# Optimization experiments

Hardware: AMD Instinct MI355X
Metric: run time of the kernel (lower is better)

Reference implementation:

```python
import jax, jax.numpy as jnp
import numpy as np

B, T, C, H = 2, 2048, 1024, 16
D = C // H  # head_dim = 64

def setup_inputs() -> dict:
    key = jax.random.key(0)
    k1, k2, k3, k4, k5 = jax.random.split(key, 5)
    x = jax.random.normal(k1, (B, T, C), dtype=jnp.float32)
    # RoPE tables (realistic frequencies)
    inv_freq = 1.0 / (10000.0 ** (jnp.arange(0, D // 2, dtype=jnp.float32) / (D // 2)))
    pos = jnp.arange(T, dtype=jnp.float32)
    ang = pos[:, None] * inv_freq[None, :]          # (T, D/2)
    cos, sin = jnp.cos(ang), jnp.sin(ang)
    # causal mask (True = keep)
    mask = jnp.tril(jnp.ones((T, T), dtype=bool))
    W_qkv = jax.random.normal(k2, (3 * C, C), dtype=jnp.float32) * (1.0 / np.sqrt(C))
    W_out = jax.random.normal(k3, (C, C), dtype=jnp.float32) * (1.0 / np.sqrt(C))
    return {"x": x, "cos": cos, "sin": sin, "mask": mask, "W_qkv": W_qkv, "W_out": W_out}

def apply_rope(x, cos, sin):
    # x: (B, H, T, D); cos/sin: (T, D/2)
    d = x.shape[-1] // 2
    x1, x2 = x[..., :d], x[..., d:]
    c = cos[None, None, :x.shape[2], :]
    s = sin[None, None, :x.shape[2], :]
    return jnp.concatenate([x1 * c - x2 * s, x2 * c + x1 * s], axis=-1)

def reference(x, cos, sin, mask, W_qkv, W_out):
    b, t, c = x.shape
    qkv = (x @ W_qkv.T).reshape(b, t, 3, H, D)
    q, k, v = qkv[:, :, 0], qkv[:, :, 1], qkv[:, :, 2]   # (b, t, H, D)
    q = q.transpose(0, 2, 1, 3)
    k = k.transpose(0, 2, 1, 3)
    v = v.transpose(0, 2, 1, 3)                           # (b, H, t, D)
    q = apply_rope(q, cos, sin)
    k = apply_rope(k, cos, sin)
    attn = jnp.einsum('bhqd,bhkd->bhqk', q, k) / jnp.sqrt(jnp.asarray(D, x.dtype))
    attn = jnp.where(mask[None, None, :, :], attn, -jnp.inf)
    attn = jax.nn.softmax(attn, axis=-1)
    out = jnp.einsum('bhqk,bhkd->bhqd', attn, v)          # (b, H, t, D)
    out = out.transpose(0, 2, 1, 3).reshape(b, t, c)
    return out @ W_out.T
```

## Files before the change

### kernel.cpp

```cpp
#include <hip/hip_runtime.h>
#include <stdint.h>

typedef __bf16 bf16;
typedef __bf16 bf16x4 __attribute__((ext_vector_type(4)));
typedef __bf16 bf16x8 __attribute__((ext_vector_type(8)));
typedef float f32x4 __attribute__((ext_vector_type(4)));

#define TSEQ 2048
#define NHEAD 16
#define HDIM 64
#define CDIM 1024

#define AS1(p) ((const __attribute__((address_space(1))) void*)(p))
#define AS3(p) ((__attribute__((address_space(3))) void*)(p))

#if __has_builtin(__builtin_amdgcn_exp2f)
#define EXP2(x) __builtin_amdgcn_exp2f(x)
#else
#define EXP2(x) exp2f(x)
#endif

__global__ __launch_bounds__(256) void cast3_bf16(const float* __restrict__ in1, int n1,
                                                  const float* __restrict__ in2, int n2,
                                                  const float* __restrict__ in3, int n3,
                                                  bf16* __restrict__ out1,
                                                  bf16* __restrict__ out2,
                                                  bf16* __restrict__ out3) {
  int i = (blockIdx.x * 256 + threadIdx.x) * 8;
  const float* src;
  bf16* dst;
  if (i < n1) {
    src = in1 + i; dst = out1 + i;
  } else if (i < n1 + n2) {
    src = in2 + (i - n1); dst = out2 + (i - n1);
  } else if (i < n1 + n2 + n3) {
    src = in3 + (i - n1 - n2); dst = out3 + (i - n1 - n2);
  } else {
    return;
  }
  float4 a = *(const float4*)src;
  float4 b = *(const float4*)(src + 4);
  bf16x8 r;
  r[0] = (bf16)a.x; r[1] = (bf16)a.y; r[2] = (bf16)a.z; r[3] = (bf16)a.w;
  r[4] = (bf16)b.x; r[5] = (bf16)b.y; r[6] = (bf16)b.z; r[7] = (bf16)b.w;
  *(bf16x8*)dst = r;
}

__global__ __launch_bounds__(256) void gemm_qkv_rope(const bf16* __restrict__ A,
                                                     const bf16* __restrict__ B,
                                                     const float* __restrict__ cosb,
                                                     const float* __restrict__ sinb,
                                                     bf16* __restrict__ Qb,
                                                     bf16* __restrict__ Kb,
                                                     bf16* __restrict__ Vt) {
  constexpr int K = 1024;
  __shared__ bf16 smem[8704];
  const int t = threadIdx.x;
  const int w = t >> 6, l = t & 63, g = l >> 4, ln = l & 15;
  const int wm = (w >> 1) * 64, wn = (w & 1) * 64;
  const int m0 = blockIdx.x * 128, n0 = blockIdx.y * 128;
  const int r0 = t >> 2, kc0 = (t & 3) * 8;

  f32x4 acc[4][4] = {};

  for (int k0 = 0; k0 < K; k0 += 32) {
    __syncthreads();
    __builtin_amdgcn_global_load_lds(AS1(A + (size_t)(m0 + r0) * K + k0 + kc0),
                                     AS3(&smem[t * 8]), 16, 0, 0);
    __builtin_amdgcn_global_load_lds(AS1(A + (size_t)(m0 + r0 + 64) * K + k0 + kc0),
                                     AS3(&smem[(t + 256) * 8]), 16, 0, 0);
    __builtin_amdgcn_global_load_lds(AS1(B + (size_t)(n0 + r0) * K + k0 + kc0),
                                     AS3(&smem[4096 + t * 8]), 16, 0, 0);
    __builtin_amdgcn_global_load_lds(AS1(B + (size_t)(n0 + r0 + 64) * K + k0 + kc0),
                                     AS3(&smem[4096 + (t + 256) * 8]), 16, 0, 0);
    __syncthreads();
    bf16x8 af[4], bfr[4];
#pragma unroll
    for (int i = 0; i < 4; i++) {
      af[i] = *(const bf16x8*)&smem[(wm + i * 16 + ln) * 32 + g * 8];
      bfr[i] = *(const bf16x8*)&smem[4096 + (wn + i * 16 + ln) * 32 + g * 8];
    }
#pragma unroll
    for (int i = 0; i < 4; i++)
#pragma unroll
      for (int j = 0; j < 4; j++)
        acc[i][j] = __builtin_amdgcn_mfma_f32_16x16x32_bf16(af[i], bfr[j], acc[i][j], 0, 0, 0);
  }

  const int part = n0 >> 10;
  if (part < 2) {
    bf16* dst = part ? Kb : Qb;
    const float qs = part ? 1.0f : 0.18033688011112042f;
#pragma unroll
    for (int i = 0; i < 4; i++)
#pragma unroll
      for (int j = 0; j < 2; j++) {
        int nl = (n0 & 1023) + wn + j * 16 + ln;
        int h = nl >> 6, d = nl & 31;
#pragma unroll
        for (int r = 0; r < 4; r++) {
          int row = m0 + wm + i * 16 + g * 4 + r;
          int tok = row & (TSEQ - 1), bb = row >> 11;
          float c = cosb[tok * 32 + d], s = sinb[tok * 32 + d];
          float a1 = acc[i][j][r], a2 = acc[i][j + 2][r];
          size_t ob = ((size_t)(bb * NHEAD + h) * TSEQ + tok) * HDIM + d;
          dst[ob] = (bf16)((a1 * c - a2 * s) * qs);
          dst[ob + 32] = (bf16)((a2 * c + a1 * s) * qs);
        }
      }
  } else {
    const int bb = m0 >> 11;
    const int tbase = m0 & (TSEQ - 1);
    const int nbase = n0 - 2048;
#pragma unroll
    for (int pass = 0; pass < 2; pass++) {
      __syncthreads();
      if ((w >> 1) == pass) {
#pragma unroll
        for (int i = 0; i < 4; i++)
#pragma unroll
          for (int j = 0; j < 4; j++) {
            int lr = i * 16 + g * 4;
            int lc = wn + j * 16 + ln;
#pragma unroll
            for (int r = 0; r < 4; r++)
              smem[(lr + r) * 132 + lc] = (bf16)acc[i][j][r];
          }
      }
      __syncthreads();
      for (int c = t; c < 1024; c += 256) {
        int ch = c >> 3, tc = c & 7;
        bf16x8 o;
#pragma unroll
        for (int j2 = 0; j2 < 8; j2++) o[j2] = smem[(tc * 8 + j2) * 132 + ch];
        int n = nbase + ch;
        int h = n >> 6, d = n & 63;
        *(bf16x8*)(Vt + ((size_t)((bb * NHEAD + h) * HDIM + d)) * TSEQ +
                   tbase + pass * 64 + tc * 8) = o;
      }
    }
  }
}

__global__ __launch_bounds__(256) void gemm_out(const bf16* __restrict__ A,
                                                const bf16* __restrict__ B,
                                                float* __restrict__ C,
                                                int M, int N, int K) {
  __shared__ bf16 As[64 * 32];
  __shared__ bf16 Bs[128 * 32];
  const int t = threadIdx.x;
  const int w = t >> 6, l = t & 63, g = l >> 4, ln = l & 15;
  const int m0 = blockIdx.x * 64, n0 = blockIdx.y * 128;
  const int r0 = t >> 2, kc0 = (t & 3) * 8;

  f32x4 acc[4][2] = {};

  for (int k0 = 0; k0 < K; k0 += 32) {
    __syncthreads();
    __builtin_amdgcn_global_load_lds(AS1(A + (size_t)(m0 + r0) * K + k0 + kc0),
                                     AS3(&As[t * 8]), 16, 0, 0);
    __builtin_amdgcn_global_load_lds(AS1(B + (size_t)(n0 + r0) * K + k0 + kc0),
                                     AS3(&Bs[t * 8]), 16, 0, 0);
    __builtin_amdgcn_global_load_lds(AS1(B + (size_t)(n0 + r0 + 64) * K + k0 + kc0),
                                     AS3(&Bs[(t + 256) * 8]), 16, 0, 0);
    __syncthreads();
    bf16x8 af[4], bfr[2];
#pragma unroll
    for (int i = 0; i < 4; i++)
      af[i] = *(const bf16x8*)&As[(i * 16 + ln) * 32 + g * 8];
#pragma unroll
    for (int j = 0; j < 2; j++)
      bfr[j] = *(const bf16x8*)&Bs[(w * 32 + j * 16 + ln) * 32 + g * 8];
#pragma unroll
    for (int i = 0; i < 4; i++)
#pragma unroll
      for (int j = 0; j < 2; j++)
        acc[i][j] = __builtin_amdgcn_mfma_f32_16x16x32_bf16(af[i], bfr[j], acc[i][j], 0, 0, 0);
  }
#pragma unroll
  for (int i = 0; i < 4; i++)
#pragma unroll
    for (int j = 0; j < 2; j++) {
      int row = m0 + i * 16 + g * 4;
      int col = n0 + w * 32 + j * 16 + ln;
#pragma unroll
      for (int r = 0; r < 4; r++)
        C[(size_t)(row + r) * N + col] = acc[i][j][r];
    }
}

__global__ __launch_bounds__(256) void attn_fwd(const bf16* __restrict__ Q,
                                                const bf16* __restrict__ K,
                                                const bf16* __restrict__ Vt,
                                                bf16* __restrict__ ctx) {
  __shared__ bf16 Ks[2][64 * 64];
  __shared__ bf16 VTs[2][64 * 64];
  __shared__ bf16 Ps[4][2][16 * 64];

  const int t = threadIdx.x;
  const int w = t >> 6;
  const int l = t & 63, g = l >> 4, ln = l & 15;
  const int bid = blockIdx.x;
  const int bh = bid & 31;
  const int qb0 = 15 - (bid >> 5);
  const size_t base = (size_t)bh * TSEQ * HDIM;

  const int q0 = qb0 * 128;
  const int qwb = q0 + w * 32;
  const int dtile = qwb >> 6;
  const int ktmax = 2 * qb0 + 1;
  const int lswz = (ln & 7) * 8;

  const int r0 = t >> 3, ch0 = (t & 7) * 8;
  const int sx = ((t & 7) ^ (r0 & 7)) * 8;
  const int s0 = r0 * 64 + sx;
  const int s1 = (r0 + 32) * 64 + sx;

  bf16x8 bq[2][2];
#pragma unroll
  for (int qs = 0; qs < 2; qs++) {
    const int q_g = qwb + qs * 16 + ln;
    bq[qs][0] = *(const bf16x8*)(Q + base + (size_t)q_g * HDIM + g * 8);
    bq[qs][1] = *(const bf16x8*)(Q + base + (size_t)q_g * HDIM + 32 + g * 8);
  }

  const bf16* kp0 = K + base + (size_t)r0 * HDIM + ch0;
  const bf16* kp1 = kp0 + 32 * HDIM;
  const bf16* vp0 = Vt + base + (size_t)r0 * TSEQ + ch0;
  const bf16* vp1 = vp0 + 32 * TSEQ;
  bf16x8 kr0 = *(const bf16x8*)kp0;
  bf16x8 kr1 = *(const bf16x8*)kp1;
  bf16x8 vr0 = *(const bf16x8*)vp0;
  bf16x8 vr1 = *(const bf16x8*)vp1;

  f32x4 acc[2][4] = {};
  float l_run[2] = {0.f, 0.f};

  for (int kt = 0; kt <= ktmax; kt++) {
    bf16* ks = Ks[kt & 1];
    bf16* vs = VTs[kt & 1];
    *(bf16x8*)&ks[s0] = kr0;
    *(bf16x8*)&ks[s1] = kr1;
    *(bf16x8*)&vs[s0] = vr0;
    *(bf16x8*)&vs[s1] = vr1;
    __syncthreads();
    if (kt < ktmax) {
      kr0 = *(const bf16x8*)(kp0 + (size_t)(kt + 1) * 64 * HDIM);
      kr1 = *(const bf16x8*)(kp1 + (size_t)(kt + 1) * 64 * HDIM);
      vr0 = *(const bf16x8*)(vp0 + (kt + 1) * 64);
      vr1 = *(const bf16x8*)(vp1 + (kt + 1) * 64);
    }
    if (kt <= dtile) {
      f32x4 st[2][4] = {};
      __builtin_amdgcn_s_setprio(1);
#pragma unroll
      for (int step = 0; step < 2; step++)
#pragma unroll
        for (int mt = 0; mt < 4; mt++) {
          bf16x8 ak = *(const bf16x8*)&ks[(mt * 16 + ln) * 64 + ((step * 32 + g * 8) ^ lswz)];
          st[0][mt] = __builtin_amdgcn_mfma_f32_16x16x32_bf16(ak, bq[0][step], st[0][mt], 0, 0, 0);
          st[1][mt] = __builtin_amdgcn_mfma_f32_16x16x32_bf16(ak, bq[1][step], st[1][mt], 0, 0, 0);
        }
      __builtin_amdgcn_s_setprio(0);
#pragma unroll
      for (int qs2 = 0; qs2 < 2; qs2++) {
        const int q_g = qwb + qs2 * 16 + ln;
        float vals[16];
        if (kt == dtile) {
#pragma unroll
          for (int mt = 0; mt < 4; mt++)
#pragma unroll
            for (int r = 0; r < 4; r++) {
              int kg = kt * 64 + mt * 16 + g * 4 + r;
              vals[mt * 4 + r] = (kg <= q_g) ? st[qs2][mt][r] : -INFINITY;
            }
        } else {
#pragma unroll
          for (int mt = 0; mt < 4; mt++)
#pragma unroll
            for (int r = 0; r < 4; r++) vals[mt * 4 + r] = st[qs2][mt][r];
        }
        float psum = 0.f;
#pragma unroll
        for (int i2 = 0; i2 < 16; i2++) {
          float p = EXP2(vals[i2]);
          vals[i2] = p;
          psum += p;
        }
        psum += __shfl_xor(psum, 16);
        psum += __shfl_xor(psum, 32);
        l_run[qs2] += psum;
#pragma unroll
        for (int mt = 0; mt < 4; mt++) {
          bf16x4 pk;
#pragma unroll
          for (int r = 0; r < 4; r++) pk[r] = (bf16)vals[mt * 4 + r];
          *(bf16x4*)&Ps[w][qs2][ln * 64 + (((mt * 16 + (g >> 1) * 8) ^ lswz) + (g & 1) * 4)] = pk;
        }
      }
      __builtin_amdgcn_s_setprio(1);
#pragma unroll
      for (int step = 0; step < 2; step++) {
        bf16x8 ap0 = *(const bf16x8*)&Ps[w][0][ln * 64 + ((step * 32 + g * 8) ^ lswz)];
        bf16x8 ap1 = *(const bf16x8*)&Ps[w][1][ln * 64 + ((step * 32 + g * 8) ^ lswz)];
#pragma unroll
        for (int nt = 0; nt < 4; nt++) {
          bf16x8 bv = *(const bf16x8*)&vs[(nt * 16 + ln) * 64 + ((step * 32 + g * 8) ^ lswz)];
          acc[0][nt] = __builtin_amdgcn_mfma_f32_16x16x32_bf16(ap0, bv, acc[0][nt], 0, 0, 0);
          acc[1][nt] = __builtin_amdgcn_mfma_f32_16x16x32_bf16(ap1, bv, acc[1][nt], 0, 0, 0);
        }
      }
      __builtin_amdgcn_s_setprio(0);
    }
  }

  const int b = bh >> 4, h = bh & (NHEAD - 1);
#pragma unroll
  for (int qs2 = 0; qs2 < 2; qs2++) {
    float inv = 1.0f / l_run[qs2];
    float lrow[4];
#pragma unroll
    for (int r = 0; r < 4; r++) lrow[r] = __shfl(inv, g * 4 + r, 64);
#pragma unroll
    for (int nt = 0; nt < 4; nt++)
#pragma unroll
      for (int r = 0; r < 4; r++) {
        int q = qwb + qs2 * 16 + g * 4 + r;
        ctx[(size_t)(b * TSEQ + q) * CDIM + h * HDIM + nt * 16 + ln] =
            (bf16)(acc[qs2][nt][r] * lrow[r]);
      }
  }
}

extern "C" void kernel_launch(void* const* d_in, const int* in_sizes, int n_in,
                              void* d_out, int out_size, void* d_ws, size_t ws_size,
                              hipStream_t stream) {
  const float* x = (const float*)d_in[0];
  const float* cosb = (const float*)d_in[1];
  const float* sinb = (const float*)d_in[2];
  const float* Wqkv = (const float*)d_in[4];
  const float* Wout = (const float*)d_in[5];
  float* out = (float*)d_out;

  char* ws = (char*)d_ws;
  bf16* x_bf = (bf16*)ws;
  bf16* ctx = (bf16*)ws;
  bf16* Wqkv_bf = (bf16*)(ws + 8388608);
  bf16* Wout_bf = (bf16*)(ws + 14680064);
  bf16* Qb = (bf16*)(ws + 16777216);
  bf16* Kb = (bf16*)(ws + 25165824);
  bf16* Vt = (bf16*)(ws + 33554432);

  cast3_bf16<<<(4194304 + 3145728 + 1048576) / 8 / 256, 256, 0, stream>>>(
      x, 4194304, Wqkv, 3145728, Wout, 1048576, x_bf, Wqkv_bf, Wout_bf);
  gemm_qkv_rope<<<dim3(32, 24), 256, 0, stream>>>(x_bf, Wqkv_bf, cosb, sinb, Qb, Kb, Vt);
  attn_fwd<<<512, 256, 0, stream>>>(Qb, Kb, Vt, ctx);
  gemm_out<<<dim3(64, 8), 256, 0, stream>>>(ctx, Wout_bf, out, 4096, 1024, 1024);
}
```

Baseline: 196.3 us.

## Split attention KV loop across two wave groups per block and merge partials

The attention block grows from 256 to 512 threads. Two groups of four waves each process alternating 64-key tiles, so each block loads 128 keys per iteration into single-buffered shared memory. At the end the second group writes its partial accumulators and row sums to shared memory, and the first group adds them, normalizes and writes the output. The goal is to halve the serial key-loop length per query tile and raise wave parallelism. The cost is an extra barrier per iteration, losing the double buffer, 64KB of shared memory per block, and a reduction epilogue.

```diff
diff --git a/kernel.cpp b/kernel.cpp
--- a/kernel.cpp
+++ b/kernel.cpp
@@ -189,16 +189,21 @@
     }
 }
 
-__global__ __launch_bounds__(256) void attn_fwd(const bf16* __restrict__ Q,
-                                                const bf16* __restrict__ K,
-                                                const bf16* __restrict__ Vt,
-                                                bf16* __restrict__ ctx) {
-  __shared__ bf16 Ks[2][64 * 64];
-  __shared__ bf16 VTs[2][64 * 64];
-  __shared__ bf16 Ps[4][2][16 * 64];
+__global__ __launch_bounds__(512, 4) void attn_fwd(const bf16* __restrict__ Q,
+                                                   const bf16* __restrict__ K,
+                                                   const bf16* __restrict__ Vt,
+                                                   bf16* __restrict__ ctx) {
+  __shared__ __align__(16) char smem_raw[65536];
+  bf16* Ks = (bf16*)smem_raw;
+  bf16* VTs = (bf16*)(smem_raw + 16384);
+  bf16* Ps = (bf16*)(smem_raw + 32768);
+  float* Mbuf = (float*)smem_raw;
+  float* Lbuf = (float*)(smem_raw + 32768);
 
   const int t = threadIdx.x;
   const int w = t >> 6;
+  const int p = w >> 2;
+  const int qw = w & 3;
   const int l = t & 63, g = l >> 4, ln = l & 15;
   const int bid = blockIdx.x;
   const int bh = bid & 31;
@@ -206,13 +211,14 @@
   const size_t base = (size_t)bh * TSEQ * HDIM;
 
   const int q0 = qb0 * 128;
-  const int qwb = q0 + w * 32;
+  const int qwb = q0 + qw * 32;
   const int dtile = qwb >> 6;
-  const int ktmax = 2 * qb0 + 1;
   const int lswz = (ln & 7) * 8;
 
-  const int r0 = t >> 3, ch0 = (t & 7) * 8;
-  const int sx = ((t & 7) ^ (r0 & 7)) * 8;
+  const int ts = t >> 8;
+  const int tt = t & 255;
+  const int r0 = tt >> 3, ch0 = (tt & 7) * 8;
+  const int sx = ((tt & 7) ^ (r0 & 7)) * 8;
   const int s0 = r0 * 64 + sx;
   const int s1 = (r0 + 32) * 64 + sx;
 
@@ -224,9 +230,9 @@
     bq[qs][1] = *(const bf16x8*)(Q + base + (size_t)q_g * HDIM + 32 + g * 8);
   }
 
-  const bf16* kp0 = K + base + (size_t)r0 * HDIM + ch0;
+  const bf16* kp0 = K + base + (size_t)(ts * 64 + r0) * HDIM + ch0;
   const bf16* kp1 = kp0 + 32 * HDIM;
-  const bf16* vp0 = Vt + base + (size_t)r0 * TSEQ + ch0;
+  const bf16* vp0 = Vt + base + (size_t)r0 * TSEQ + ts * 64 + ch0;
   const bf16* vp1 = vp0 + 32 * TSEQ;
   bf16x8 kr0 = *(const bf16x8*)kp0;
   bf16x8 kr1 = *(const bf16x8*)kp1;
@@ -236,20 +242,20 @@
   f32x4 acc[2][4] = {};
   float l_run[2] = {0.f, 0.f};
 
-  for (int kt = 0; kt <= ktmax; kt++) {
-    bf16* ks = Ks[kt & 1];
-    bf16* vs = VTs[kt & 1];
-    *(bf16x8*)&ks[s0] = kr0;
-    *(bf16x8*)&ks[s1] = kr1;
-    *(bf16x8*)&vs[s0] = vr0;
-    *(bf16x8*)&vs[s1] = vr1;
-    __syncthreads();
-    if (kt < ktmax) {
-      kr0 = *(const bf16x8*)(kp0 + (size_t)(kt + 1) * 64 * HDIM);
-      kr1 = *(const bf16x8*)(kp1 + (size_t)(kt + 1) * 64 * HDIM);
-      vr0 = *(const bf16x8*)(vp0 + (kt + 1) * 64);
-      vr1 = *(const bf16x8*)(vp1 + (kt + 1) * 64);
-    }
+  for (int i = 0; i <= qb0; i++) {
+    __syncthreads();
+    *(bf16x8*)&Ks[ts * 4096 + s0] = kr0;
+    *(bf16x8*)&Ks[ts * 4096 + s1] = kr1;
+    *(bf16x8*)&VTs[ts * 4096 + s0] = vr0;
+    *(bf16x8*)&VTs[ts * 4096 + s1] = vr1;
+    __syncthreads();
+    if (i < qb0) {
+      kr0 = *(const bf16x8*)(kp0 + (size_t)(i + 1) * 128 * HDIM);
+      kr1 = *(const bf16x8*)(kp1 + (size_t)(i + 1) * 128 * HDIM);
+      vr0 = *(const bf16x8*)(vp0 + (i + 1) * 128);
+      vr1 = *(const bf16x8*)(vp1 + (i + 1) * 128);
+    }
+    const int kt = 2 * i + p;
     if (kt <= dtile) {
       f32x4 st[2][4] = {};
       __builtin_amdgcn_s_setprio(1);
@@ -257,7 +263,8 @@
       for (int step = 0; step < 2; step++)
 #pragma unroll
         for (int mt = 0; mt < 4; mt++) {
-          bf16x8 ak = *(const bf16x8*)&ks[(mt * 16 + ln) * 64 + ((step * 32 + g * 8) ^ lswz)];
+          bf16x8 ak = *(const bf16x8*)&Ks[p * 4096 + (mt * 16 + ln) * 64 +
+                                          ((step * 32 + g * 8) ^ lswz)];
           st[0][mt] = __builtin_amdgcn_mfma_f32_16x16x32_bf16(ak, bq[0][step], st[0][mt], 0, 0, 0);
           st[1][mt] = __builtin_amdgcn_mfma_f32_16x16x32_bf16(ak, bq[1][step], st[1][mt], 0, 0, 0);
         }
@@ -283,9 +290,9 @@
         float psum = 0.f;
 #pragma unroll
         for (int i2 = 0; i2 < 16; i2++) {
-          float p = EXP2(vals[i2]);
-          vals[i2] = p;
-          psum += p;
+          float pv = EXP2(vals[i2]);
+          vals[i2] = pv;
+          psum += pv;
         }
         psum += __shfl_xor(psum, 16);
         psum += __shfl_xor(psum, 32);
@@ -295,17 +302,21 @@
           bf16x4 pk;
 #pragma unroll
           for (int r = 0; r < 4; r++) pk[r] = (bf16)vals[mt * 4 + r];
-          *(bf16x4*)&Ps[w][qs2][ln * 64 + (((mt * 16 + (g >> 1) * 8) ^ lswz) + (g & 1) * 4)] = pk;
+          *(bf16x4*)&Ps[(w * 2 + qs2) * 1024 + ln * 64 +
+                        (((mt * 16 + (g >> 1) * 8) ^ lswz) + (g & 1) * 4)] = pk;
         }
       }
       __builtin_amdgcn_s_setprio(1);
 #pragma unroll
       for (int step = 0; step < 2; step++) {
-        bf16x8 ap0 = *(const bf16x8*)&Ps[w][0][ln * 64 + ((step * 32 + g * 8) ^ lswz)];
-        bf16x8 ap1 = *(const bf16x8*)&Ps[w][1][ln * 64 + ((step * 32 + g * 8) ^ lswz)];
+        bf16x8 ap0 = *(const bf16x8*)&Ps[(w * 2 + 0) * 1024 + ln * 64 +
+                                         ((step * 32 + g * 8) ^ lswz)];
+        bf16x8 ap1 = *(const bf16x8*)&Ps[(w * 2 + 1) * 1024 + ln * 64 +
+                                         ((step * 32 + g * 8) ^ lswz)];
 #pragma unroll
         for (int nt = 0; nt < 4; nt++) {
-          bf16x8 bv = *(const bf16x8*)&vs[(nt * 16 + ln) * 64 + ((step * 32 + g * 8) ^ lswz)];
+          bf16x8 bv = *(const bf16x8*)&VTs[p * 4096 + (nt * 16 + ln) * 64 +
+                                           ((step * 32 + g * 8) ^ lswz)];
           acc[0][nt] = __builtin_amdgcn_mfma_f32_16x16x32_bf16(ap0, bv, acc[0][nt], 0, 0, 0);
           acc[1][nt] = __builtin_amdgcn_mfma_f32_16x16x32_bf16(ap1, bv, acc[1][nt], 0, 0, 0);
         }
@@ -314,21 +325,38 @@
     }
   }
 
-  const int b = bh >> 4, h = bh & (NHEAD - 1);
-#pragma unroll
-  for (int qs2 = 0; qs2 < 2; qs2++) {
-    float inv = 1.0f / l_run[qs2];
-    float lrow[4];
-#pragma unroll
-    for (int r = 0; r < 4; r++) lrow[r] = __shfl(inv, g * 4 + r, 64);
-#pragma unroll
-    for (int nt = 0; nt < 4; nt++)
-#pragma unroll
-      for (int r = 0; r < 4; r++) {
-        int q = qwb + qs2 * 16 + g * 4 + r;
-        ctx[(size_t)(b * TSEQ + q) * CDIM + h * HDIM + nt * 16 + ln] =
-            (bf16)(acc[qs2][nt][r] * lrow[r]);
-      }
+  __syncthreads();
+  if (p == 1) {
+#pragma unroll
+    for (int qs2 = 0; qs2 < 2; qs2++) {
+#pragma unroll
+      for (int nt = 0; nt < 4; nt++)
+        *(f32x4*)&Mbuf[(qw * 64 + l) * 32 + qs2 * 16 + nt * 4] = acc[qs2][nt];
+      Lbuf[(qw * 64 + l) * 2 + qs2] = l_run[qs2];
+    }
+  }
+  __syncthreads();
+  if (p == 0) {
+    const int b = bh >> 4, h = bh & (NHEAD - 1);
+#pragma unroll
+    for (int qs2 = 0; qs2 < 2; qs2++) {
+#pragma unroll
+      for (int nt = 0; nt < 4; nt++)
+        acc[qs2][nt] += *(const f32x4*)&Mbuf[(qw * 64 + l) * 32 + qs2 * 16 + nt * 4];
+      float lt = l_run[qs2] + Lbuf[(qw * 64 + l) * 2 + qs2];
+      float inv = 1.0f / lt;
+      float lrow[4];
+#pragma unroll
+      for (int r = 0; r < 4; r++) lrow[r] = __shfl(inv, g * 4 + r, 64);
+#pragma unroll
+      for (int nt = 0; nt < 4; nt++)
+#pragma unroll
+        for (int r = 0; r < 4; r++) {
+          int q = qwb + qs2 * 16 + g * 4 + r;
+          ctx[(size_t)(b * TSEQ + q) * CDIM + h * HDIM + nt * 16 + ln] =
+              (bf16)(acc[qs2][nt][r] * lrow[r]);
+        }
+    }
   }
 }
 
@@ -354,6 +382,6 @@
   cast3_bf16<<<(4194304 + 3145728 + 1048576) / 8 / 256, 256, 0, stream>>>(
       x, 4194304, Wqkv, 3145728, Wout, 1048576, x_bf, Wqkv_bf, Wout_bf);
   gemm_qkv_rope<<<dim3(32, 24), 256, 0, stream>>>(x_bf, Wqkv_bf, cosb, sinb, Qb, Kb, Vt);
-  attn_fwd<<<512, 256, 0, stream>>>(Qb, Kb, Vt, ctx);
+  attn_fwd<<<512, 512, 0, stream>>>(Qb, Kb, Vt, ctx);
   gemm_out<<<dim3(64, 8), 256, 0, stream>>>(ctx, Wout_bf, out, 4096, 1024, 1024);
 }
```

Measured after the change: 199.7 us. Within noise of the previous version (+1.7%).
